# Performance work log

Measured on AMD Instinct MI355X. Metric: run time of the kernel, lower is better.

The kernel has to match this reference:

```python
import jax, jax.numpy as jnp
import numpy as np

B, IN, H, T = 4096, 1024, 1024, 12
TIME_PENALTY = 0.01
PONDER_EPS = 0.01


def lstm_cell(x, h, c, Wih, Whh, bih, bhh):
    # PyTorch LSTMCell: gates ordered i, f, g, o
    g = x @ Wih.T + bih + h @ Whh.T + bhh  # [B, 4H]
    i, f, gg, o = jnp.split(g, 4, axis=1)
    i = jax.nn.sigmoid(i)
    f = jax.nn.sigmoid(f)
    gg = jnp.tanh(gg)
    o = jax.nn.sigmoid(o)
    c_new = f * c + i * gg
    h_new = o * jnp.tanh(c_new)
    return h_new, c_new


def setup_inputs() -> dict:
    key = jax.random.key(0)
    ks = jax.random.split(key, 12)
    k1 = 1.0 / np.sqrt(H)
    u = lambda k, shape: jax.random.uniform(k, shape, jnp.float32, -k1, k1)
    return {
        "inputs": jax.random.normal(ks[0], (B, IN), jnp.float32),
        "W_ih1": u(ks[1], (4 * H, IN + 1)),
        "W_hh1": u(ks[2], (4 * H, H)),
        "b_ih1": u(ks[3], (4 * H,)),
        "b_hh1": u(ks[4], (4 * H,)),
        "W_ih2": u(ks[5], (4 * H, H)),
        "W_hh2": u(ks[6], (4 * H, H)),
        "b_ih2": u(ks[7], (4 * H,)),
        "b_hh2": u(ks[8], (4 * H,)),
        "W_halt": u(ks[9], (1, H)),
        "b_halt": jnp.full((1,), -1.0, jnp.float32),  # initial_halting_bias
    }


def reference(inputs, W_ih1, W_hh1, b_ih1, b_hh1, W_ih2, W_hh2, b_ih2, b_hh2, W_halt, b_halt):
    batch = inputs.shape[0]
    budget = jnp.float32(1.0 - PONDER_EPS)

    h1 = jnp.zeros((batch, H), jnp.float32)
    c1 = jnp.zeros((batch, H), jnp.float32)
    h2 = jnp.zeros((batch, H), jnp.float32)
    c2 = jnp.zeros((batch, H), jnp.float32)
    halt_accum = jnp.zeros((batch, 1), jnp.float32)
    acc_out = jnp.zeros((batch, H), jnp.float32)
    acc_rem = jnp.zeros((batch, 1), jnp.float32)
    ponder_steps = jnp.zeros((batch,), jnp.float32)
    cont = jnp.ones((batch, 1), bool)
    is_first = jnp.array(True)

    def step(carry, _):
        h1, c1, h2, c2, halt_accum, acc_out, acc_rem, ponder_steps, cont, is_first = carry
        active = jnp.any(cont)  # mimic torch's early break: inactive steps are no-ops
        flag = jnp.where(is_first, 1.0, 0.0) * jnp.ones((batch, 1), jnp.float32)
        x = jnp.concatenate([inputs, flag], axis=1)
        h1n, c1n = lstm_cell(x, h1, c1, W_ih1, W_hh1, b_ih1, b_hh1)
        act = jax.nn.relu(h1n)
        h2n, c2n = lstm_cell(act, h2, c2, W_ih2, W_hh2, b_ih2, b_hh2)
        step_halt = jax.nn.sigmoid(h2n @ W_halt.T + b_halt)  # [B,1]
        cont_f = cont.astype(jnp.float32)
        masked_halt = step_halt * cont_f
        halt_n = halt_accum + masked_halt
        ending = (halt_n > budget) & cont
        cont_n = cont & jnp.logical_not(ending)
        masked_rem = ending.astype(jnp.float32) * (1.0 - halt_n)
        acc_out_n = acc_out + (masked_halt + masked_rem) * h2n
        acc_rem_n = acc_rem + masked_halt
        ponder_n = ponder_steps + cont_n[:, 0].astype(jnp.float32)
        sel = lambda new, old: jnp.where(active, new, old)
        carry_n = (sel(h1n, h1), sel(c1n, c1), sel(h2n, h2), sel(c2n, c2),
                   sel(halt_n, halt_accum), sel(acc_out_n, acc_out),
                   sel(acc_rem_n, acc_rem), sel(ponder_n, ponder_steps),
                   jnp.where(active, cont_n, cont),
                   is_first & jnp.logical_not(active))
        return carry_n, None

    carry = (h1, c1, h2, c2, halt_accum, acc_out, acc_rem, ponder_steps, cont, is_first)
    carry, _ = jax.lax.scan(step, carry, None, length=T)
    h1, c1, h2, c2, halt_accum, acc_out, acc_rem, ponder_steps, cont, _ = carry

    # for-else branch: samples still continuing after time_limit get the remainder
    acc_out = acc_out + cont.astype(jnp.float32) * (1.0 - halt_accum) * h2
    ponder_cost = -1.0 * TIME_PENALTY * jnp.mean(acc_rem)
    return acc_out, h1, c1, h2, c2, ponder_cost, ponder_steps
```

## Files before the change

### kernel.cpp

```cpp
#include <hip/hip_runtime.h>
#include <cstdint>
#include <cstddef>


typedef _Float16 f16;
typedef f16   f16x8 __attribute__((ext_vector_type(8)));
typedef f16   f16x4 __attribute__((ext_vector_type(4)));
typedef float f32x4 __attribute__((ext_vector_type(4)));

#define TSTEPS 12

#define O_ACC   0u
#define O_H1    4194304u
#define O_C1    8388608u
#define O_H2    12582912u
#define O_C2    16777216u
#define O_PCOST 20971520u
#define O_PSTEP 20971521u

#define WS_C1    ((size_t)0u)
#define WS_C2    ((size_t)16u<<20)
#define WS_H1HI  ((size_t)32u<<20)
#define WS_H1LO  ((size_t)40u<<20)
#define WS_H2HI  ((size_t)48u<<20)
#define WS_H2LO  ((size_t)56u<<20)
#define WS_ACTHI ((size_t)64u<<20)
#define WS_ACTLO ((size_t)72u<<20)
#define WS_W2HI  ((size_t)80u<<20)
#define WS_W2LO  ((size_t)88u<<20)
#define WS_W3HI  ((size_t)96u<<20)
#define WS_W3LO  ((size_t)104u<<20)
#define WS_MISC  ((size_t)112u<<20)

#define SEC_ALO 32768
#define BUFSZ   65536

__device__ __forceinline__ float sigmoidf_(float x) { return 1.0f / (1.0f + expf(-x)); }

__device__ __forceinline__ void glds16(const void* g, void* l) {
    __builtin_amdgcn_global_load_lds(
        (const __attribute__((address_space(1))) unsigned int*)g,
        (__attribute__((address_space(3))) unsigned int*)l, 16, 0, 0);
}

__device__ __forceinline__ void block_tile(int& m0, int& hc0) {
    const int bid = blockIdx.x;
    const int lid = (bid & 7) * 32 + (bid >> 3);
    m0  = (lid & 15) * 256;
    hc0 = (lid >> 4) * 64;
}

template<bool B_PAIR>
__device__ __forceinline__ void passK64(
    const f16* __restrict__ Ahi, const f16* __restrict__ Alo,
    const f16* __restrict__ Bhi, const f16* __restrict__ Blo,
    const float* __restrict__ Bf32,
    int m0, int hc0, f32x4 (&acc)[8][4], char* sm)
{
    const int tid = threadIdx.x, lane = tid & 63, wid = tid >> 6;
    const int wm  = (wid >> 2) * 128;
    const int wnb = wid & 3;
    const int l15 = lane & 15, lk = lane >> 4;

    int rbase[8], rx[8];
#pragma unroll
    for (int mf = 0; mf < 8; ++mf) {
        const int row = wm + mf * 16 + l15;
        rbase[mf] = row * 128;
        rx[mf]    = row & 7;
    }

    const int secA = wid >> 2;
    const int j0   = (wid & 3) * 8;
    const int rl = lane >> 3, sl = lane & 7;
    const f16* gaBase = (secA ? Alo : Ahi)
                        + (size_t)(m0 + j0 * 8 + rl) * 1024 + ((sl ^ rl) << 3);
    const int albase0 = secA * SEC_ALO + j0 * 1024;

    const int wrow0 = hc0 + wnb * 16 + l15;
    const float* pB32 = nullptr;
    const f16* pBh = nullptr;
    const f16* pBl = nullptr;
    if constexpr (B_PAIR) {
        pBh = Bhi + (size_t)wrow0 * 1024 + lk * 8;
        pBl = Blo + (size_t)wrow0 * 1024 + lk * 8;
    } else {
        pB32 = Bf32 + (size_t)wrow0 * 1024 + lk * 8;
    }

    f16x8 bh0[4], bl0[4], bh1[4], bl1[4];
    float4 P[8];

    auto issueA = [&](int kt, char* buf) {
#pragma unroll
        for (int i = 0; i < 8; ++i)
            glds16(gaBase + (size_t)i * 8192 + kt * 64, buf + albase0 + i * 1024);
    };
    auto loadBP = [&](int kt, int ks, f16x8 (&H)[4], f16x8 (&L)[4]) {
#pragma unroll
        for (int nf = 0; nf < 4; ++nf) {
            H[nf] = *(const f16x8*)(pBh + (size_t)nf * 1048576 + kt * 64 + ks * 32);
            L[nf] = *(const f16x8*)(pBl + (size_t)nf * 1048576 + kt * 64 + ks * 32);
        }
    };
    auto loadBM = [&](int kt, int ks) {
#pragma unroll
        for (int nf = 0; nf < 4; ++nf) {
            const float* p = pB32 + (size_t)nf * 1048576 + kt * 64 + ks * 32;
            P[2 * nf]     = *(const float4*)(p);
            P[2 * nf + 1] = *(const float4*)(p + 4);
        }
    };
    auto cvtM = [&](f16x8 (&H)[4], f16x8 (&L)[4]) {
#pragma unroll
        for (int nf = 0; nf < 4; ++nf) {
            const float* f0 = (const float*)&P[2 * nf];
            const float* f1 = (const float*)&P[2 * nf + 1];
            f16x8 h, l;
#pragma unroll
            for (int j = 0; j < 4; ++j) {
                const f16 a = (f16)f0[j];
                h[j] = a; l[j] = (f16)(f0[j] - (float)a);
                const f16 b = (f16)f1[j];
                h[4 + j] = b; l[4 + j] = (f16)(f1[j] - (float)b);
            }
            H[nf] = h; L[nf] = l;
        }
    };
    auto cluster = [&](const f16x8 (&BH)[4], const f16x8 (&BL)[4], int ks, char* bc) {
#pragma unroll
        for (int mg = 0; mg < 4; ++mg) {
            const int o0 = rbase[2 * mg]     + ((((ks << 2) | lk) ^ rx[2 * mg])     << 4);
            const int o1 = rbase[2 * mg + 1] + ((((ks << 2) | lk) ^ rx[2 * mg + 1]) << 4);
            const f16x8 ah0 = *(const f16x8*)(bc + o0);
            const f16x8 al0 = *(const f16x8*)(bc + SEC_ALO + o0);
            const f16x8 ah1 = *(const f16x8*)(bc + o1);
            const f16x8 al1 = *(const f16x8*)(bc + SEC_ALO + o1);
            __builtin_amdgcn_s_setprio(1);
#pragma unroll
            for (int nf = 0; nf < 4; ++nf) {
                acc[2 * mg][nf]     = __builtin_amdgcn_mfma_f32_16x16x32_f16(ah0, BH[nf], acc[2 * mg][nf], 0, 0, 0);
                acc[2 * mg + 1][nf] = __builtin_amdgcn_mfma_f32_16x16x32_f16(ah1, BH[nf], acc[2 * mg + 1][nf], 0, 0, 0);
            }
#pragma unroll
            for (int nf = 0; nf < 4; ++nf) {
                acc[2 * mg][nf]     = __builtin_amdgcn_mfma_f32_16x16x32_f16(ah0, BL[nf], acc[2 * mg][nf], 0, 0, 0);
                acc[2 * mg + 1][nf] = __builtin_amdgcn_mfma_f32_16x16x32_f16(ah1, BL[nf], acc[2 * mg + 1][nf], 0, 0, 0);
            }
#pragma unroll
            for (int nf = 0; nf < 4; ++nf) {
                acc[2 * mg][nf]     = __builtin_amdgcn_mfma_f32_16x16x32_f16(al0, BH[nf], acc[2 * mg][nf], 0, 0, 0);
                acc[2 * mg + 1][nf] = __builtin_amdgcn_mfma_f32_16x16x32_f16(al1, BH[nf], acc[2 * mg + 1][nf], 0, 0, 0);
            }
            __builtin_amdgcn_s_setprio(0);
        }
    };

    if constexpr (B_PAIR) loadBP(0, 0, bh0, bl0);
    else                  loadBM(0, 0);
    issueA(0, sm);
    asm volatile("s_waitcnt vmcnt(0)" ::: "memory");
    __builtin_amdgcn_s_barrier();
    asm volatile("" ::: "memory");

#pragma unroll 1
    for (int kt = 0; kt < 16; ++kt) {
        char* bc = sm + (kt & 1) * BUFSZ;
        char* bn = sm + ((kt + 1) & 1) * BUFSZ;
        const bool pre = (kt < 15);

        if constexpr (B_PAIR) {
            loadBP(kt, 1, bh1, bl1);
            if (pre) issueA(kt + 1, bn);
            cluster(bh0, bl0, 0, bc);
            if (pre) asm volatile("s_waitcnt vmcnt(8)" ::: "memory");
            else     asm volatile("s_waitcnt vmcnt(0)" ::: "memory");
            if (pre) loadBP(kt + 1, 0, bh0, bl0);
            cluster(bh1, bl1, 1, bc);
        } else {
            cvtM(bh0, bl0);
            loadBM(kt, 1);
            if (pre) issueA(kt + 1, bn);
            cluster(bh0, bl0, 0, bc);
            if (pre) asm volatile("s_waitcnt vmcnt(8)" ::: "memory");
            else     asm volatile("s_waitcnt vmcnt(0)" ::: "memory");
            cvtM(bh0, bl0);
            if (pre) loadBM(kt + 1, 0);
            cluster(bh0, bl0, 1, bc);
        }
        asm volatile("s_waitcnt vmcnt(0)" ::: "memory");
        if (pre) {
            __builtin_amdgcn_s_barrier();
            asm volatile("" ::: "memory");
        }
    }
}

__global__ __launch_bounds__(512, 2) void k_z1(
    const f16* __restrict__ xhi, const f16* __restrict__ xlo,
    const f16* __restrict__ W1hi, const f16* __restrict__ W1lo,
    const float* __restrict__ bih1, const float* __restrict__ bhh1,
    float* __restrict__ Z1)
{
    __shared__ __align__(16) char sm[2 * BUFSZ];
    int m0, hc0; block_tile(m0, hc0);
    f32x4 acc[8][4];
#pragma unroll
    for (int a = 0; a < 8; ++a)
#pragma unroll
        for (int b = 0; b < 4; ++b) acc[a][b] = (f32x4){0.f, 0.f, 0.f, 0.f};
    passK64<true>(xhi, xlo, W1hi, W1lo, nullptr, m0, hc0, acc, sm);

    const int tid = threadIdx.x, lane = tid & 63, wid = tid >> 6;
    const int wm = (wid >> 2) * 128, wnb = wid & 3, l15 = lane & 15, lk = lane >> 4;
    const int hc = hc0 + wnb * 16 + l15;
#pragma unroll
    for (int mf = 0; mf < 8; ++mf)
#pragma unroll
        for (int r = 0; r < 4; ++r) {
            const int row = m0 + wm + mf * 16 + lk * 4 + r;
#pragma unroll
            for (int g = 0; g < 4; ++g) {
                const int R = g * 1024 + hc;
                Z1[(size_t)row * 4096 + R] = acc[mf][g][r] + bih1[R] + bhh1[R];
            }
        }
}

__global__ __launch_bounds__(512, 2) void k_stepA(
    const float* __restrict__ Z1, const float* __restrict__ Whh1,
    const float* __restrict__ flagcol, float* __restrict__ c1,
    f16* __restrict__ h1hi, f16* __restrict__ h1lo,
    f16* __restrict__ acthi, f16* __restrict__ actlo,
    const unsigned* __restrict__ cnt_prev, int step)
{
    if (step > 0 && cnt_prev[0] == 0u) return;
    __shared__ __align__(16) char sm[2 * BUFSZ];
    int m0, hc0; block_tile(m0, hc0);
    f32x4 acc[8][4];
#pragma unroll
    for (int a = 0; a < 8; ++a)
#pragma unroll
        for (int b = 0; b < 4; ++b) acc[a][b] = (f32x4){0.f, 0.f, 0.f, 0.f};
    if (step > 0)
        passK64<false>(h1hi, h1lo, nullptr, nullptr, Whh1, m0, hc0, acc, sm);

    const int tid = threadIdx.x, lane = tid & 63, wid = tid >> 6;
    const int wm = (wid >> 2) * 128, wnb = wid & 3, l15 = lane & 15, lk = lane >> 4;
    const int hc = hc0 + wnb * 16 + l15;
#pragma unroll
    for (int mf = 0; mf < 8; ++mf)
#pragma unroll
        for (int r = 0; r < 4; ++r) {
            const int row = m0 + wm + mf * 16 + lk * 4 + r;
            float p[4];
#pragma unroll
            for (int g = 0; g < 4; ++g) {
                const int R = g * 1024 + hc;
                p[g] = acc[mf][g][r] + Z1[(size_t)row * 4096 + R];
                if (step == 0) p[g] += flagcol[R];
            }
            const float ig = sigmoidf_(p[0]);
            const float fg = sigmoidf_(p[1]);
            const float gg = tanhf(p[2]);
            const float og = sigmoidf_(p[3]);
            const int idx = row * 1024 + hc;
            const float cold = (step == 0) ? 0.0f : c1[idx];
            const float cn = fg * cold + ig * gg;
            c1[idx] = cn;
            const float h = og * tanhf(cn);
            const f16 hh = (f16)h;
            const f16 hl = (f16)(h - (float)hh);
            h1hi[idx] = hh; h1lo[idx] = hl;
            const bool pos = h > 0.0f;
            acthi[idx] = pos ? hh : (f16)0.0f;
            actlo[idx] = pos ? hl : (f16)0.0f;
        }
}

__global__ __launch_bounds__(512, 2) void k_stepB(
    const f16* __restrict__ acthi, const f16* __restrict__ actlo,
    const f16* __restrict__ W2hi, const f16* __restrict__ W2lo,
    f16* __restrict__ h2hi, f16* __restrict__ h2lo,
    const f16* __restrict__ W3hi, const f16* __restrict__ W3lo,
    const float* __restrict__ bih2, const float* __restrict__ bhh2,
    float* __restrict__ c2,
    const unsigned* __restrict__ cnt_prev, int step)
{
    if (step > 0 && cnt_prev[0] == 0u) return;
    __shared__ __align__(16) char sm[2 * BUFSZ];
    int m0, hc0; block_tile(m0, hc0);
    f32x4 acc[8][4];
#pragma unroll
    for (int a = 0; a < 8; ++a)
#pragma unroll
        for (int b = 0; b < 4; ++b) acc[a][b] = (f32x4){0.f, 0.f, 0.f, 0.f};
    passK64<true>(acthi, actlo, W2hi, W2lo, nullptr, m0, hc0, acc, sm);
    if (step > 0)
        passK64<true>(h2hi, h2lo, W3hi, W3lo, nullptr, m0, hc0, acc, sm);

    const int tid = threadIdx.x, lane = tid & 63, wid = tid >> 6;
    const int wm = (wid >> 2) * 128, wnb = wid & 3, l15 = lane & 15, lk = lane >> 4;
    const int hc = hc0 + wnb * 16 + l15;
#pragma unroll
    for (int mf = 0; mf < 8; ++mf)
#pragma unroll
        for (int r = 0; r < 4; ++r) {
            const int row = m0 + wm + mf * 16 + lk * 4 + r;
            float p[4];
#pragma unroll
            for (int g = 0; g < 4; ++g) {
                const int R = g * 1024 + hc;
                p[g] = acc[mf][g][r] + bih2[R] + bhh2[R];
            }
            const float ig = sigmoidf_(p[0]);
            const float fg = sigmoidf_(p[1]);
            const float gg = tanhf(p[2]);
            const float og = sigmoidf_(p[3]);
            const int idx = row * 1024 + hc;
            const float cold = (step == 0) ? 0.0f : c2[idx];
            const float cn = fg * cold + ig * gg;
            c2[idx] = cn;
            const float h = og * tanhf(cn);
            const f16 hh = (f16)h;
            h2hi[idx] = hh;
            h2lo[idx] = (f16)(h - (float)hh);
        }
}

__global__ __launch_bounds__(256) void k_haltacc(
    const f16* __restrict__ h2hi, const f16* __restrict__ h2lo,
    const float* __restrict__ Whalt, const float* __restrict__ bhalt,
    float* __restrict__ halt, float* __restrict__ cont,
    float* __restrict__ ponder_out, unsigned* __restrict__ ctrl,
    float* __restrict__ acc_out,
    const unsigned* __restrict__ cnt_prev, int step)
{
    if (step > 0 && cnt_prev[0] == 0u) return;
    const int lane = threadIdx.x & 63;
    const int b = blockIdx.x * 4 + (threadIdx.x >> 6);
    const size_t base = (size_t)b * 1024;
    float sum = 0.0f;
    for (int k = lane; k < 1024; k += 64)
        sum += ((float)h2hi[base + k] + (float)h2lo[base + k]) * Whalt[k];
#pragma unroll
    for (int off = 32; off > 0; off >>= 1) sum += __shfl_down(sum, off, 64);
    float co = 0.0f;
    if (lane == 0) {
        const float sh = sigmoidf_(sum + bhalt[0]);
        if (cont[b] != 0.0f) {
            const float hn = halt[b] + sh;
            const bool ending = hn > 0.99f;
            co = sh + (ending ? (1.0f - hn) : 0.0f);
            halt[b] = hn;
            if (!ending) {
                ponder_out[b] += 1.0f;
                atomicAdd(&ctrl[step], 1u);
            } else {
                cont[b] = 0.0f;
            }
        }
    }
    co = __shfl(co, 0, 64);
    if (step == 0 || co != 0.0f) {
        float4* dst = (float4*)(acc_out + base);
        const f16x4* hi4 = (const f16x4*)(h2hi + base);
        const f16x4* lo4 = (const f16x4*)(h2lo + base);
#pragma unroll
        for (int j = 0; j < 4; ++j) {
            const int i = lane + 64 * j;
            const f16x4 hv = hi4[i];
            const f16x4 lv = lo4[i];
            float4 d = (step == 0) ? (float4){0.f, 0.f, 0.f, 0.f} : dst[i];
            d.x = fmaf(co, (float)hv[0] + (float)lv[0], d.x);
            d.y = fmaf(co, (float)hv[1] + (float)lv[1], d.y);
            d.z = fmaf(co, (float)hv[2] + (float)lv[2], d.z);
            d.w = fmaf(co, (float)hv[3] + (float)lv[3], d.w);
            dst[i] = d;
        }
    }
}

__global__ __launch_bounds__(256) void k_small_init(
    float* __restrict__ halt, float* __restrict__ cont,
    float* __restrict__ ponder_out, unsigned* __restrict__ ctrl)
{
    const int b = blockIdx.x * 256 + threadIdx.x;
    if (b < 4096) { halt[b] = 0.0f; cont[b] = 1.0f; ponder_out[b] = 0.0f; }
    if (b < 16) ctrl[b] = 0u;
}

__global__ __launch_bounds__(256) void k_split_flat(
    const float* __restrict__ src, f16* __restrict__ hi, f16* __restrict__ lo)
{
    const size_t i = ((size_t)blockIdx.x * 256 + threadIdx.x) * 4;
    const float4 v = *(const float4*)(src + i);
    const f16 s0 = (f16)v.x, s1 = (f16)v.y, s2 = (f16)v.z, s3 = (f16)v.w;
    const f16x4 hv = {s0, s1, s2, s3};
    const f16x4 lw = {(f16)(v.x - (float)s0), (f16)(v.y - (float)s1),
                      (f16)(v.z - (float)s2), (f16)(v.w - (float)s3)};
    *(f16x4*)(hi + i) = hv;
    *(f16x4*)(lo + i) = lw;
}

__global__ __launch_bounds__(256) void k_split_wih1(
    const float* __restrict__ src, f16* __restrict__ hi, f16* __restrict__ lo,
    float* __restrict__ flagcol)
{
    const int t = blockIdx.x * 256 + threadIdx.x;
    const int row = t >> 8, c4 = (t & 255) << 2;
    const float* s = src + (size_t)row * 1025 + c4;
    const float v0 = s[0], v1 = s[1], v2 = s[2], v3 = s[3];
    const f16 s0 = (f16)v0, s1 = (f16)v1, s2 = (f16)v2, s3 = (f16)v3;
    const f16x4 hv = {s0, s1, s2, s3};
    const f16x4 lw = {(f16)(v0 - (float)s0), (f16)(v1 - (float)s1),
                      (f16)(v2 - (float)s2), (f16)(v3 - (float)s3)};
    const size_t di = (size_t)row * 1024 + c4;
    *(f16x4*)(hi + di) = hv;
    *(f16x4*)(lo + di) = lw;
    if ((t & 255) == 0) flagcol[row] = src[(size_t)row * 1025 + 1024];
}

__global__ __launch_bounds__(256) void k_fin1(
    const f16* __restrict__ h1hi, const f16* __restrict__ h1lo,
    const f16* __restrict__ h2hi, const f16* __restrict__ h2lo,
    const float* __restrict__ c1s, const float* __restrict__ c2s,
    const float* __restrict__ halt, const float* __restrict__ cont,
    float* __restrict__ out)
{
    const int b = blockIdx.x;
    const float rem = (cont[b] != 0.0f) ? (1.0f - halt[b]) : 0.0f;
    const int base = b * 1024;
    for (int i = threadIdx.x; i < 1024; i += 256) {
        const float h1v = (float)h1hi[base + i] + (float)h1lo[base + i];
        const float h2v = (float)h2hi[base + i] + (float)h2lo[base + i];
        out[O_H1 + base + i] = h1v;
        out[O_C1 + base + i] = c1s[base + i];
        out[O_H2 + base + i] = h2v;
        out[O_C2 + base + i] = c2s[base + i];
        if (rem != 0.0f) out[O_ACC + base + i] += rem * h2v;
    }
}

__global__ __launch_bounds__(256) void k_fin2(
    const float* __restrict__ halt, float* __restrict__ out)
{
    __shared__ float red[256];
    float s = 0.0f;
    for (int i = threadIdx.x; i < 4096; i += 256) s += halt[i];
    red[threadIdx.x] = s;
    __syncthreads();
    for (int w = 128; w > 0; w >>= 1) {
        if (threadIdx.x < w) red[threadIdx.x] += red[threadIdx.x + w];
        __syncthreads();
    }
    if (threadIdx.x == 0) out[O_PCOST] = -0.01f * (red[0] * (1.0f / 4096.0f));
}

extern "C" void kernel_launch(void* const* d_in, const int* in_sizes, int n_in,
                              void* d_out, int out_size, void* d_ws, size_t ws_size,
                              hipStream_t stream) {
    const float* inputs = (const float*)d_in[0];
    const float* W_ih1  = (const float*)d_in[1];
    const float* W_hh1  = (const float*)d_in[2];
    const float* b_ih1  = (const float*)d_in[3];
    const float* b_hh1  = (const float*)d_in[4];
    const float* W_ih2  = (const float*)d_in[5];
    const float* W_hh2  = (const float*)d_in[6];
    const float* b_ih2  = (const float*)d_in[7];
    const float* b_hh2  = (const float*)d_in[8];
    const float* W_halt = (const float*)d_in[9];
    const float* b_halt = (const float*)d_in[10];

    float* out = (float*)d_out;
    float* Z1  = out + O_H1;

    char* wsb = (char*)d_ws;
    float* c1s = (float*)(wsb + WS_C1);
    float* c2s = (float*)(wsb + WS_C2);
    f16* h1hi = (f16*)(wsb + WS_H1HI);
    f16* h1lo = (f16*)(wsb + WS_H1LO);
    f16* h2hi = (f16*)(wsb + WS_H2HI);
    f16* h2lo = (f16*)(wsb + WS_H2LO);
    f16* acthi = (f16*)(wsb + WS_ACTHI);
    f16* actlo = (f16*)(wsb + WS_ACTLO);
    f16* W2hi = (f16*)(wsb + WS_W2HI);
    f16* W2lo = (f16*)(wsb + WS_W2LO);
    f16* W3hi = (f16*)(wsb + WS_W3HI);
    f16* W3lo = (f16*)(wsb + WS_W3LO);
    float* halt    = (float*)(wsb + WS_MISC);
    float* cont    = halt + 4096;
    float* flagcol = cont + 4096;
    unsigned* ctrl = (unsigned*)(flagcol + 4096);

    f16* xhi  = h1hi; f16* xlo  = h1lo;
    f16* W1hi = h2hi; f16* W1lo = h2lo;

    k_small_init<<<16, 256, 0, stream>>>(halt, cont, out + O_PSTEP, ctrl);

    k_split_wih1<<<4096, 256, 0, stream>>>(W_ih1, W1hi, W1lo, flagcol);
    k_split_flat<<<4096, 256, 0, stream>>>(inputs, xhi, xlo);
    k_split_flat<<<4096, 256, 0, stream>>>(W_ih2, W2hi, W2lo);
    k_split_flat<<<4096, 256, 0, stream>>>(W_hh2, W3hi, W3lo);
    k_z1<<<256, 512, 0, stream>>>(xhi, xlo, W1hi, W1lo, b_ih1, b_hh1, Z1);

    for (int s = 0; s < TSTEPS; ++s) {
        const unsigned* cnt_prev = ctrl + (s > 0 ? s - 1 : 0);

        k_stepA<<<256, 512, 0, stream>>>(Z1, W_hh1, flagcol, c1s,
                                         h1hi, h1lo, acthi, actlo,
                                         cnt_prev, s);
        k_stepB<<<256, 512, 0, stream>>>(acthi, actlo, W2hi, W2lo,
                                         h2hi, h2lo, W3hi, W3lo,
                                         b_ih2, b_hh2, c2s,
                                         cnt_prev, s);
        k_haltacc<<<1024, 256, 0, stream>>>(h2hi, h2lo, W_halt, b_halt,
                                            halt, cont, out + O_PSTEP, ctrl,
                                            out + O_ACC, cnt_prev, s);
    }

    k_fin1<<<4096, 256, 0, stream>>>(h1hi, h1lo, h2hi, h2lo,
                                     c1s, c2s, halt, cont, out);
    k_fin2<<<1, 256, 0, stream>>>(halt, out);
}
```

Before: 1.533 ms.

## Halve GEMM block M-tile to 128 rows and launch twice as many blocks

The block tile shrinks from 256x64 to 128x64, which halves LDS buffers and accumulator registers. Grids double to 512 blocks and launch bounds allow 4 blocks per CU, so all 256 CUs get work with more waves resident. The B-operand register double-buffering across k-substeps is removed: B fragments are now loaded inline per n-pair right before their MFMAs. This exposes global-load latency in exchange for lower register pressure, and each B fragment is reused across fewer A rows, so weight traffic goes up.

Result: slower. 1.880 ms (+22.6%).

```diff
diff --git a/kernel.cpp b/kernel.cpp
--- a/kernel.cpp
+++ b/kernel.cpp
@@ -32,8 +32,8 @@
 #define WS_W3LO  ((size_t)104u<<20)
 #define WS_MISC  ((size_t)112u<<20)
 
-#define SEC_ALO 32768
-#define BUFSZ   65536
+#define SEC_ALO 16384
+#define BUFSZ   32768
 
 __device__ __forceinline__ float sigmoidf_(float x) { return 1.0f / (1.0f + expf(-x)); }
 
@@ -45,9 +45,9 @@
 
 __device__ __forceinline__ void block_tile(int& m0, int& hc0) {
     const int bid = blockIdx.x;
-    const int lid = (bid & 7) * 32 + (bid >> 3);
-    m0  = (lid & 15) * 256;
-    hc0 = (lid >> 4) * 64;
+    const int lid = (bid & 7) * 64 + (bid >> 3);
+    m0  = (lid & 31) * 128;
+    hc0 = (lid >> 5) * 64;
 }
 
 template<bool B_PAIR>
@@ -55,27 +55,27 @@
     const f16* __restrict__ Ahi, const f16* __restrict__ Alo,
     const f16* __restrict__ Bhi, const f16* __restrict__ Blo,
     const float* __restrict__ Bf32,
-    int m0, int hc0, f32x4 (&acc)[8][4], char* sm)
+    int m0, int hc0, f32x4 (&acc)[4][4], char* sm)
 {
     const int tid = threadIdx.x, lane = tid & 63, wid = tid >> 6;
-    const int wm  = (wid >> 2) * 128;
+    const int wm  = (wid >> 2) * 64;
     const int wnb = wid & 3;
     const int l15 = lane & 15, lk = lane >> 4;
 
-    int rbase[8], rx[8];
-#pragma unroll
-    for (int mf = 0; mf < 8; ++mf) {
+    int rbase[4], rx[4];
+#pragma unroll
+    for (int mf = 0; mf < 4; ++mf) {
         const int row = wm + mf * 16 + l15;
         rbase[mf] = row * 128;
         rx[mf]    = row & 7;
     }
 
     const int secA = wid >> 2;
-    const int j0   = (wid & 3) * 8;
+    const int j0   = (wid & 3) * 4;
     const int rl = lane >> 3, sl = lane & 7;
     const f16* gaBase = (secA ? Alo : Ahi)
                         + (size_t)(m0 + j0 * 8 + rl) * 1024 + ((sl ^ rl) << 3);
-    const int albase0 = secA * SEC_ALO + j0 * 1024;
+    const int lb0 = secA * SEC_ALO + j0 * 1024;
 
     const int wrow0 = hc0 + wnb * 16 + l15;
     const float* pB32 = nullptr;
@@ -88,76 +88,12 @@
         pB32 = Bf32 + (size_t)wrow0 * 1024 + lk * 8;
     }
 
-    f16x8 bh0[4], bl0[4], bh1[4], bl1[4];
-    float4 P[8];
-
     auto issueA = [&](int kt, char* buf) {
 #pragma unroll
-        for (int i = 0; i < 8; ++i)
-            glds16(gaBase + (size_t)i * 8192 + kt * 64, buf + albase0 + i * 1024);
+        for (int i = 0; i < 4; ++i)
+            glds16(gaBase + (size_t)i * 8192 + kt * 64, buf + lb0 + i * 1024);
     };
-    auto loadBP = [&](int kt, int ks, f16x8 (&H)[4], f16x8 (&L)[4]) {
-#pragma unroll
-        for (int nf = 0; nf < 4; ++nf) {
-            H[nf] = *(const f16x8*)(pBh + (size_t)nf * 1048576 + kt * 64 + ks * 32);
-            L[nf] = *(const f16x8*)(pBl + (size_t)nf * 1048576 + kt * 64 + ks * 32);
-        }
-    };
-    auto loadBM = [&](int kt, int ks) {
-#pragma unroll
-        for (int nf = 0; nf < 4; ++nf) {
-            const float* p = pB32 + (size_t)nf * 1048576 + kt * 64 + ks * 32;
-            P[2 * nf]     = *(const float4*)(p);
-            P[2 * nf + 1] = *(const float4*)(p + 4);
-        }
-    };
-    auto cvtM = [&](f16x8 (&H)[4], f16x8 (&L)[4]) {
-#pragma unroll
-        for (int nf = 0; nf < 4; ++nf) {
-            const float* f0 = (const float*)&P[2 * nf];
-            const float* f1 = (const float*)&P[2 * nf + 1];
-            f16x8 h, l;
-#pragma unroll
-            for (int j = 0; j < 4; ++j) {
-                const f16 a = (f16)f0[j];
-                h[j] = a; l[j] = (f16)(f0[j] - (float)a);
-                const f16 b = (f16)f1[j];
-                h[4 + j] = b; l[4 + j] = (f16)(f1[j] - (float)b);
-            }
-            H[nf] = h; L[nf] = l;
-        }
-    };
-    auto cluster = [&](const f16x8 (&BH)[4], const f16x8 (&BL)[4], int ks, char* bc) {
-#pragma unroll
-        for (int mg = 0; mg < 4; ++mg) {
-            const int o0 = rbase[2 * mg]     + ((((ks << 2) | lk) ^ rx[2 * mg])     << 4);
-            const int o1 = rbase[2 * mg + 1] + ((((ks << 2) | lk) ^ rx[2 * mg + 1]) << 4);
-            const f16x8 ah0 = *(const f16x8*)(bc + o0);
-            const f16x8 al0 = *(const f16x8*)(bc + SEC_ALO + o0);
-            const f16x8 ah1 = *(const f16x8*)(bc + o1);
-            const f16x8 al1 = *(const f16x8*)(bc + SEC_ALO + o1);
-            __builtin_amdgcn_s_setprio(1);
-#pragma unroll
-            for (int nf = 0; nf < 4; ++nf) {
-                acc[2 * mg][nf]     = __builtin_amdgcn_mfma_f32_16x16x32_f16(ah0, BH[nf], acc[2 * mg][nf], 0, 0, 0);
-                acc[2 * mg + 1][nf] = __builtin_amdgcn_mfma_f32_16x16x32_f16(ah1, BH[nf], acc[2 * mg + 1][nf], 0, 0, 0);
-            }
-#pragma unroll
-            for (int nf = 0; nf < 4; ++nf) {
-                acc[2 * mg][nf]     = __builtin_amdgcn_mfma_f32_16x16x32_f16(ah0, BL[nf], acc[2 * mg][nf], 0, 0, 0);
-                acc[2 * mg + 1][nf] = __builtin_amdgcn_mfma_f32_16x16x32_f16(ah1, BL[nf], acc[2 * mg + 1][nf], 0, 0, 0);
-            }
-#pragma unroll
-            for (int nf = 0; nf < 4; ++nf) {
-                acc[2 * mg][nf]     = __builtin_amdgcn_mfma_f32_16x16x32_f16(al0, BH[nf], acc[2 * mg][nf], 0, 0, 0);
-                acc[2 * mg + 1][nf] = __builtin_amdgcn_mfma_f32_16x16x32_f16(al1, BH[nf], acc[2 * mg + 1][nf], 0, 0, 0);
-            }
-            __builtin_amdgcn_s_setprio(0);
-        }
-    };
-
-    if constexpr (B_PAIR) loadBP(0, 0, bh0, bl0);
-    else                  loadBM(0, 0);
+
     issueA(0, sm);
     asm volatile("s_waitcnt vmcnt(0)" ::: "memory");
     __builtin_amdgcn_s_barrier();
@@ -167,36 +103,70 @@
     for (int kt = 0; kt < 16; ++kt) {
         char* bc = sm + (kt & 1) * BUFSZ;
         char* bn = sm + ((kt + 1) & 1) * BUFSZ;
-        const bool pre = (kt < 15);
-
-        if constexpr (B_PAIR) {
-            loadBP(kt, 1, bh1, bl1);
-            if (pre) issueA(kt + 1, bn);
-            cluster(bh0, bl0, 0, bc);
-            if (pre) asm volatile("s_waitcnt vmcnt(8)" ::: "memory");
-            else     asm volatile("s_waitcnt vmcnt(0)" ::: "memory");
-            if (pre) loadBP(kt + 1, 0, bh0, bl0);
-            cluster(bh1, bl1, 1, bc);
-        } else {
-            cvtM(bh0, bl0);
-            loadBM(kt, 1);
-            if (pre) issueA(kt + 1, bn);
-            cluster(bh0, bl0, 0, bc);
-            if (pre) asm volatile("s_waitcnt vmcnt(8)" ::: "memory");
-            else     asm volatile("s_waitcnt vmcnt(0)" ::: "memory");
-            cvtM(bh0, bl0);
-            if (pre) loadBM(kt + 1, 0);
-            cluster(bh0, bl0, 1, bc);
+        if (kt < 15) issueA(kt + 1, bn);
+
+#pragma unroll
+        for (int ks = 0; ks < 2; ++ks) {
+#pragma unroll
+            for (int np = 0; np < 2; ++np) {
+                f16x8 bh[2], bl[2];
+#pragma unroll
+                for (int q = 0; q < 2; ++q) {
+                    const size_t bo = (size_t)(2 * np + q) * 1048576 + kt * 64 + ks * 32;
+                    if constexpr (B_PAIR) {
+                        bh[q] = *(const f16x8*)(pBh + bo);
+                        bl[q] = *(const f16x8*)(pBl + bo);
+                    } else {
+                        const float* p = pB32 + bo;
+                        const float4 v0 = *(const float4*)(p);
+                        const float4 v1 = *(const float4*)(p + 4);
+                        const float f[8] = {v0.x, v0.y, v0.z, v0.w, v1.x, v1.y, v1.z, v1.w};
+                        f16x8 h, l;
+#pragma unroll
+                        for (int j = 0; j < 8; ++j) {
+                            const f16 a = (f16)f[j];
+                            h[j] = a; l[j] = (f16)(f[j] - (float)a);
+                        }
+                        bh[q] = h; bl[q] = l;
+                    }
+                }
+#pragma unroll
+                for (int mg = 0; mg < 2; ++mg) {
+                    const int o0 = rbase[2 * mg]     + ((((ks << 2) | lk) ^ rx[2 * mg])     << 4);
+                    const int o1 = rbase[2 * mg + 1] + ((((ks << 2) | lk) ^ rx[2 * mg + 1]) << 4);
+                    const f16x8 ah0 = *(const f16x8*)(bc + o0);
+                    const f16x8 al0 = *(const f16x8*)(bc + SEC_ALO + o0);
+                    const f16x8 ah1 = *(const f16x8*)(bc + o1);
+                    const f16x8 al1 = *(const f16x8*)(bc + SEC_ALO + o1);
+                    __builtin_amdgcn_s_setprio(1);
+#pragma unroll
+                    for (int q = 0; q < 2; ++q) {
+                        acc[2 * mg][2 * np + q]     = __builtin_amdgcn_mfma_f32_16x16x32_f16(ah0, bh[q], acc[2 * mg][2 * np + q], 0, 0, 0);
+                        acc[2 * mg + 1][2 * np + q] = __builtin_amdgcn_mfma_f32_16x16x32_f16(ah1, bh[q], acc[2 * mg + 1][2 * np + q], 0, 0, 0);
+                    }
+#pragma unroll
+                    for (int q = 0; q < 2; ++q) {
+                        acc[2 * mg][2 * np + q]     = __builtin_amdgcn_mfma_f32_16x16x32_f16(ah0, bl[q], acc[2 * mg][2 * np + q], 0, 0, 0);
+                        acc[2 * mg + 1][2 * np + q] = __builtin_amdgcn_mfma_f32_16x16x32_f16(ah1, bl[q], acc[2 * mg + 1][2 * np + q], 0, 0, 0);
+                    }
+#pragma unroll
+                    for (int q = 0; q < 2; ++q) {
+                        acc[2 * mg][2 * np + q]     = __builtin_amdgcn_mfma_f32_16x16x32_f16(al0, bh[q], acc[2 * mg][2 * np + q], 0, 0, 0);
+                        acc[2 * mg + 1][2 * np + q] = __builtin_amdgcn_mfma_f32_16x16x32_f16(al1, bh[q], acc[2 * mg + 1][2 * np + q], 0, 0, 0);
+                    }
+                    __builtin_amdgcn_s_setprio(0);
+                }
+            }
         }
         asm volatile("s_waitcnt vmcnt(0)" ::: "memory");
-        if (pre) {
+        if (kt < 15) {
             __builtin_amdgcn_s_barrier();
             asm volatile("" ::: "memory");
         }
     }
 }
 
-__global__ __launch_bounds__(512, 2) void k_z1(
+__global__ __launch_bounds__(512, 4) void k_z1(
     const f16* __restrict__ xhi, const f16* __restrict__ xlo,
     const f16* __restrict__ W1hi, const f16* __restrict__ W1lo,
     const float* __restrict__ bih1, const float* __restrict__ bhh1,
@@ -204,18 +174,18 @@
 {
     __shared__ __align__(16) char sm[2 * BUFSZ];
     int m0, hc0; block_tile(m0, hc0);
-    f32x4 acc[8][4];
-#pragma unroll
-    for (int a = 0; a < 8; ++a)
+    f32x4 acc[4][4];
+#pragma unroll
+    for (int a = 0; a < 4; ++a)
 #pragma unroll
         for (int b = 0; b < 4; ++b) acc[a][b] = (f32x4){0.f, 0.f, 0.f, 0.f};
     passK64<true>(xhi, xlo, W1hi, W1lo, nullptr, m0, hc0, acc, sm);
 
     const int tid = threadIdx.x, lane = tid & 63, wid = tid >> 6;
-    const int wm = (wid >> 2) * 128, wnb = wid & 3, l15 = lane & 15, lk = lane >> 4;
+    const int wm = (wid >> 2) * 64, wnb = wid & 3, l15 = lane & 15, lk = lane >> 4;
     const int hc = hc0 + wnb * 16 + l15;
 #pragma unroll
-    for (int mf = 0; mf < 8; ++mf)
+    for (int mf = 0; mf < 4; ++mf)
 #pragma unroll
         for (int r = 0; r < 4; ++r) {
             const int row = m0 + wm + mf * 16 + lk * 4 + r;
@@ -227,7 +197,7 @@
         }
 }
 
-__global__ __launch_bounds__(512, 2) void k_stepA(
+__global__ __launch_bounds__(512, 4) void k_stepA(
     const float* __restrict__ Z1, const float* __restrict__ Whh1,
     const float* __restrict__ flagcol, float* __restrict__ c1,
     f16* __restrict__ h1hi, f16* __restrict__ h1lo,
@@ -237,19 +207,19 @@
     if (step > 0 && cnt_prev[0] == 0u) return;
     __shared__ __align__(16) char sm[2 * BUFSZ];
     int m0, hc0; block_tile(m0, hc0);
-    f32x4 acc[8][4];
-#pragma unroll
-    for (int a = 0; a < 8; ++a)
+    f32x4 acc[4][4];
+#pragma unroll
+    for (int a = 0; a < 4; ++a)
 #pragma unroll
         for (int b = 0; b < 4; ++b) acc[a][b] = (f32x4){0.f, 0.f, 0.f, 0.f};
     if (step > 0)
         passK64<false>(h1hi, h1lo, nullptr, nullptr, Whh1, m0, hc0, acc, sm);
 
     const int tid = threadIdx.x, lane = tid & 63, wid = tid >> 6;
-    const int wm = (wid >> 2) * 128, wnb = wid & 3, l15 = lane & 15, lk = lane >> 4;
+    const int wm = (wid >> 2) * 64, wnb = wid & 3, l15 = lane & 15, lk = lane >> 4;
     const int hc = hc0 + wnb * 16 + l15;
 #pragma unroll
-    for (int mf = 0; mf < 8; ++mf)
+    for (int mf = 0; mf < 4; ++mf)
 #pragma unroll
         for (int r = 0; r < 4; ++r) {
             const int row = m0 + wm + mf * 16 + lk * 4 + r;
@@ -278,7 +248,7 @@
         }
 }
 
-__global__ __launch_bounds__(512, 2) void k_stepB(
+__global__ __launch_bounds__(512, 4) void k_stepB(
     const f16* __restrict__ acthi, const f16* __restrict__ actlo,
     const f16* __restrict__ W2hi, const f16* __restrict__ W2lo,
     f16* __restrict__ h2hi, f16* __restrict__ h2lo,
@@ -290,9 +260,9 @@
     if (step > 0 && cnt_prev[0] == 0u) return;
     __shared__ __align__(16) char sm[2 * BUFSZ];
     int m0, hc0; block_tile(m0, hc0);
-    f32x4 acc[8][4];
-#pragma unroll
-    for (int a = 0; a < 8; ++a)
+    f32x4 acc[4][4];
+#pragma unroll
+    for (int a = 0; a < 4; ++a)
 #pragma unroll
         for (int b = 0; b < 4; ++b) acc[a][b] = (f32x4){0.f, 0.f, 0.f, 0.f};
     passK64<true>(acthi, actlo, W2hi, W2lo, nullptr, m0, hc0, acc, sm);
@@ -300,10 +270,10 @@
         passK64<true>(h2hi, h2lo, W3hi, W3lo, nullptr, m0, hc0, acc, sm);
 
     const int tid = threadIdx.x, lane = tid & 63, wid = tid >> 6;
-    const int wm = (wid >> 2) * 128, wnb = wid & 3, l15 = lane & 15, lk = lane >> 4;
+    const int wm = (wid >> 2) * 64, wnb = wid & 3, l15 = lane & 15, lk = lane >> 4;
     const int hc = hc0 + wnb * 16 + l15;
 #pragma unroll
-    for (int mf = 0; mf < 8; ++mf)
+    for (int mf = 0; mf < 4; ++mf)
 #pragma unroll
         for (int r = 0; r < 4; ++r) {
             const int row = m0 + wm + mf * 16 + lk * 4 + r;
@@ -502,15 +472,15 @@
     k_split_flat<<<4096, 256, 0, stream>>>(inputs, xhi, xlo);
     k_split_flat<<<4096, 256, 0, stream>>>(W_ih2, W2hi, W2lo);
     k_split_flat<<<4096, 256, 0, stream>>>(W_hh2, W3hi, W3lo);
-    k_z1<<<256, 512, 0, stream>>>(xhi, xlo, W1hi, W1lo, b_ih1, b_hh1, Z1);
+    k_z1<<<512, 512, 0, stream>>>(xhi, xlo, W1hi, W1lo, b_ih1, b_hh1, Z1);
 
     for (int s = 0; s < TSTEPS; ++s) {
         const unsigned* cnt_prev = ctrl + (s > 0 ? s - 1 : 0);
 
-        k_stepA<<<256, 512, 0, stream>>>(Z1, W_hh1, flagcol, c1s,
+        k_stepA<<<512, 512, 0, stream>>>(Z1, W_hh1, flagcol, c1s,
                                          h1hi, h1lo, acthi, actlo,
                                          cnt_prev, s);
-        k_stepB<<<256, 512, 0, stream>>>(acthi, actlo, W2hi, W2lo,
+        k_stepB<<<512, 512, 0, stream>>>(acthi, actlo, W2hi, W2lo,
                                          h2hi, h2lo, W3hi, W3lo,
                                          b_ih2, b_hh2, c2s,
                                          cnt_prev, s);
```

## Pre-pack split fp16 weights into fragment-contiguous layout for coalesced B loads

Applied to the files above, without the earlier changes.

Weight matrices are now split into hi/lo fp16 and written in a layout ordered by MFMA fragment (tile, k-tile, k-step, warp column block, n-fragment, lane). Each wave's B-operand load then reads 64 lanes × 16 bytes contiguously instead of strided rows 1024 elements apart. The aim is to improve global-load coalescing and cache-line use for the B operand in the GEMM kernels. The pack kernel itself does strided scalar reads, and the flag column extraction moves to a separate tiny kernel.

After: 1.415 ms. 1.08x faster.

```diff
diff --git a/kernel.cpp b/kernel.cpp
--- a/kernel.cpp
+++ b/kernel.cpp
@@ -77,14 +77,15 @@
                         + (size_t)(m0 + j0 * 8 + rl) * 1024 + ((sl ^ rl) << 3);
     const int albase0 = secA * SEC_ALO + j0 * 1024;
 
-    const int wrow0 = hc0 + wnb * 16 + l15;
     const float* pB32 = nullptr;
-    const f16* pBh = nullptr;
-    const f16* pBl = nullptr;
+    const f16* pwh = nullptr;
+    const f16* pwl = nullptr;
     if constexpr (B_PAIR) {
-        pBh = Bhi + (size_t)wrow0 * 1024 + lk * 8;
-        pBl = Blo + (size_t)wrow0 * 1024 + lk * 8;
+        const size_t pbase = ((size_t)((hc0 >> 6) * 512 + wnb * 4)) * 512 + (size_t)lane * 8;
+        pwh = Bhi + pbase;
+        pwl = Blo + pbase;
     } else {
+        const int wrow0 = hc0 + wnb * 16 + l15;
         pB32 = Bf32 + (size_t)wrow0 * 1024 + lk * 8;
     }
 
@@ -97,10 +98,11 @@
             glds16(gaBase + (size_t)i * 8192 + kt * 64, buf + albase0 + i * 1024);
     };
     auto loadBP = [&](int kt, int ks, f16x8 (&H)[4], f16x8 (&L)[4]) {
+        const size_t o = (size_t)kt * 16384 + (size_t)ks * 8192;
 #pragma unroll
         for (int nf = 0; nf < 4; ++nf) {
-            H[nf] = *(const f16x8*)(pBh + (size_t)nf * 1048576 + kt * 64 + ks * 32);
-            L[nf] = *(const f16x8*)(pBl + (size_t)nf * 1048576 + kt * 64 + ks * 32);
+            H[nf] = *(const f16x8*)(pwh + o + nf * 512);
+            L[nf] = *(const f16x8*)(pwl + o + nf * 512);
         }
     };
     auto loadBM = [&](int kt, int ks) {
@@ -403,22 +405,37 @@
     *(f16x4*)(lo + i) = lw;
 }
 
-__global__ __launch_bounds__(256) void k_split_wih1(
+__global__ __launch_bounds__(256) void k_pack_w(
     const float* __restrict__ src, f16* __restrict__ hi, f16* __restrict__ lo,
-    float* __restrict__ flagcol)
-{
-    const int t = blockIdx.x * 256 + threadIdx.x;
-    const int row = t >> 8, c4 = (t & 255) << 2;
-    const float* s = src + (size_t)row * 1025 + c4;
-    const float v0 = s[0], v1 = s[1], v2 = s[2], v3 = s[3];
-    const f16 s0 = (f16)v0, s1 = (f16)v1, s2 = (f16)v2, s3 = (f16)v3;
-    const f16x4 hv = {s0, s1, s2, s3};
-    const f16x4 lw = {(f16)(v0 - (float)s0), (f16)(v1 - (float)s1),
-                      (f16)(v2 - (float)s2), (f16)(v3 - (float)s3)};
-    const size_t di = (size_t)row * 1024 + c4;
-    *(f16x4*)(hi + di) = hv;
-    *(f16x4*)(lo + di) = lw;
-    if ((t & 255) == 0) flagcol[row] = src[(size_t)row * 1025 + 1024];
+    int stride)
+{
+    const size_t t = (size_t)blockIdx.x * 256 + threadIdx.x;
+    const int lane = (int)(t & 63);
+    const size_t C = t >> 6;
+    const int nf  = (int)(C & 3);
+    const int wnb = (int)((C >> 2) & 3);
+    const int ks  = (int)((C >> 4) & 1);
+    const int kt  = (int)((C >> 5) & 15);
+    const int T   = (int)(C >> 9);
+    const int row = nf * 1024 + T * 64 + wnb * 16 + (lane & 15);
+    const int k0  = kt * 64 + ks * 32 + (lane >> 4) * 8;
+    const float* s = src + (size_t)row * stride + k0;
+    f16x8 h, l;
+#pragma unroll
+    for (int j = 0; j < 8; ++j) {
+        const float v = s[j];
+        const f16 a = (f16)v;
+        h[j] = a; l[j] = (f16)(v - (float)a);
+    }
+    *(f16x8*)(hi + t * 8) = h;
+    *(f16x8*)(lo + t * 8) = l;
+}
+
+__global__ __launch_bounds__(256) void k_flagcol(
+    const float* __restrict__ Wih1, float* __restrict__ flagcol)
+{
+    const int r = blockIdx.x * 256 + threadIdx.x;
+    if (r < 4096) flagcol[r] = Wih1[(size_t)r * 1025 + 1024];
 }
 
 __global__ __launch_bounds__(256) void k_fin1(
@@ -498,10 +515,11 @@
 
     k_small_init<<<16, 256, 0, stream>>>(halt, cont, out + O_PSTEP, ctrl);
 
-    k_split_wih1<<<4096, 256, 0, stream>>>(W_ih1, W1hi, W1lo, flagcol);
+    k_flagcol<<<16, 256, 0, stream>>>(W_ih1, flagcol);
+    k_pack_w<<<2048, 256, 0, stream>>>(W_ih1, W1hi, W1lo, 1025);
+    k_pack_w<<<2048, 256, 0, stream>>>(W_ih2, W2hi, W2lo, 1024);
+    k_pack_w<<<2048, 256, 0, stream>>>(W_hh2, W3hi, W3lo, 1024);
     k_split_flat<<<4096, 256, 0, stream>>>(inputs, xhi, xlo);
-    k_split_flat<<<4096, 256, 0, stream>>>(W_ih2, W2hi, W2lo);
-    k_split_flat<<<4096, 256, 0, stream>>>(W_hh2, W3hi, W3lo);
     k_z1<<<256, 512, 0, stream>>>(xhi, xlo, W1hi, W1lo, b_ih1, b_hh1, Z1);
 
     for (int s = 0; s < TSTEPS; ++s) {
```
